# Kernel optimization log

Measured on AMD Instinct MI355X. Metric: run time of the kernel, lower is better.

The kernel has to match this reference:

```python
import jax, jax.numpy as jnp
import numpy as np

H, W = 256, 256
N = 1024
EPS2D = 1e-4  # regularizer added to 2D covariances before inversion


def setup_inputs() -> dict:
    key = jax.random.key(0)
    ks = jax.random.split(key, 6)
    xy = jax.random.normal(ks[0], (N, 2), dtype=jnp.float32) * 3.0
    z = jax.random.uniform(ks[1], (N, 1), minval=2.0, maxval=30.0, dtype=jnp.float32)
    means3D = jnp.concatenate([xy, z], axis=-1)                      # [N,3], depths in (1,50)
    A = 0.1 * jax.random.normal(ks[2], (N, 3, 3), dtype=jnp.float32)
    covs3d = A @ jnp.swapaxes(A, -1, -2) + 0.01 * jnp.eye(3, dtype=jnp.float32)  # SPD [N,3,3]
    colors = jax.random.uniform(ks[3], (N, 3), dtype=jnp.float32)
    opacities = jax.random.uniform(ks[4], (N,), dtype=jnp.float32)
    Kmat = jnp.array([[300.0, 0.0, W / 2.0], [0.0, 300.0, H / 2.0], [0.0, 0.0, 1.0]], dtype=jnp.float32)
    Rmat = jnp.eye(3, dtype=jnp.float32)
    t = jnp.zeros((3,), dtype=jnp.float32)
    return {"means3D": means3D, "covs3d": covs3d, "colors": colors,
            "opacities": opacities, "K": Kmat, "R": Rmat, "t": t}


def reference(means3D, covs3d, colors, opacities, K, R, t):
    n = means3D.shape[0]
    # ---- projection ----
    cam = means3D @ R.T + t[None, :]                      # [N,3]
    depths = jnp.maximum(cam[:, 2], 1.0)
    screen = cam @ K.T
    means2D = screen[:, :2] / screen[:, 2:3]              # [N,2]
    fx, fy = K[0, 0], K[1, 1]
    inv_z = 1.0 / cam[:, 2]
    z2 = cam[:, 2] ** 2
    zeros = jnp.zeros_like(inv_z)
    row0 = jnp.stack([inv_z * fx, zeros, -cam[:, 0] / z2 * fx], axis=-1)
    row1 = jnp.stack([zeros, inv_z * fy, -cam[:, 1] / z2 * fy], axis=-1)
    J = jnp.stack([row0, row1], axis=1)                   # [N,2,3]
    covs_cam = jnp.einsum('ij,njk,lk->nil', R, covs3d, R)  # [N,3,3]
    covs2D = jnp.einsum('nij,njk,nlk->nil', J, covs_cam, J)  # [N,2,2]

    # ---- depth sort ----
    order = jnp.argsort(depths)
    means2D = means2D[order]
    covs2D = covs2D[order]
    colors_s = colors[order]
    opac_s = opacities[order]
    depths_s = depths[order]
    valid = (depths_s > 1.0) & (depths_s < 50.0)

    # ---- per-pixel gaussian evaluation (closed-form 2x2 inverse == cholesky_inverse) ----
    covs2D = covs2D + EPS2D * jnp.eye(2, dtype=covs2D.dtype)
    a = covs2D[:, 0, 0]; b = covs2D[:, 0, 1]; c = covs2D[:, 1, 1]
    det = a * c - b * b                                   # [N]
    ia = c / det; ib = -b / det; ic = a / det

    yy, xx = jnp.meshgrid(jnp.arange(H, dtype=jnp.float32),
                          jnp.arange(W, dtype=jnp.float32), indexing='ij')
    dx0 = xx[None] - means2D[:, 0, None, None]            # [N,H,W]
    dx1 = yy[None] - means2D[:, 1, None, None]            # [N,H,W]
    q = (ia[:, None, None] * dx0 * dx0
         + 2.0 * ib[:, None, None] * dx0 * dx1
         + ic[:, None, None] * dx1 * dx1)
    gauss = jnp.exp(-0.5 * q) / (2.0 * jnp.pi * jnp.sqrt(det))[:, None, None]
    gauss = gauss * valid[:, None, None].astype(gauss.dtype)

    # ---- alpha compositing (front-to-back) ----
    alphas = opac_s[:, None, None] * gauss                # [N,H,W]
    T = jnp.cumprod(1.0 - alphas, axis=0)
    T = jnp.concatenate([jnp.ones_like(alphas[:1]), T[:-1]], axis=0)
    weights = T * alphas                                  # [N,H,W]
    rendered = jnp.einsum('nhw,nc->hwc', weights, colors_s)  # [H,W,3]
    return rendered
```

## Files before the change

kernel.cpp:

```cpp
#include <hip/hip_runtime.h>
#include <math.h>

#define HH 256
#define WW 256
#define EPS2D 1e-4f
#define MAXN 1024
#define CULL_THR 23.0f
#define NL_HALF_LOG2E -0.72134752044448170368f


__global__ __launch_bounds__(256) void prep_kernel(
    const float* __restrict__ means3D, const float* __restrict__ covs3d,
    const float* __restrict__ colors,  const float* __restrict__ opac,
    const float* __restrict__ Km,      const float* __restrict__ Rm,
    const float* __restrict__ tv,
    float4* __restrict__ A, float4* __restrict__ B, float* __restrict__ C,
    int n)
{
    __shared__ float s_mean[MAXN*3];
    __shared__ float s_depth[MAXN];
    __shared__ float s_cov[64*9];
    __shared__ float s_col[64*3];
    __shared__ float s_op[64];
    __shared__ int   s_pr[4][64];

    int t = threadIdx.x, lane = t & 63, w = t >> 6;
    int g0b = blockIdx.x * 64;
    int nb = n - g0b; if (nb > 64) nb = 64; if (nb < 0) nb = 0;

    {
        int nm4 = (3*n) >> 2;
        const float4* m4 = (const float4*)means3D;
        for (int i = t; i < nm4; i += 256) ((float4*)s_mean)[i] = m4[i];
        for (int i = (nm4<<2) + t; i < 3*n; i += 256) s_mean[i] = means3D[i];

        const float* cbase = covs3d + (size_t)g0b * 9;
        int ncf = nb * 9, nc4 = ncf >> 2;
        for (int i = t; i < nc4; i += 256) ((float4*)s_cov)[i] = ((const float4*)cbase)[i];
        for (int i = (nc4<<2) + t; i < ncf; i += 256) s_cov[i] = cbase[i];

        const float* lbase = colors + (size_t)g0b * 3;
        int nlf = nb * 3, nl4 = nlf >> 2;
        for (int i = t; i < nl4; i += 256) ((float4*)s_col)[i] = ((const float4*)lbase)[i];
        for (int i = (nl4<<2) + t; i < nlf; i += 256) s_col[i] = lbase[i];

        const float* obase = opac + g0b;
        int no4 = nb >> 2;
        for (int i = t; i < no4; i += 256) ((float4*)s_op)[i] = ((const float4*)obase)[i];
        for (int i = (no4<<2) + t; i < nb; i += 256) s_op[i] = obase[i];
    }
    __syncthreads();

    float R00=Rm[0],R01=Rm[1],R02=Rm[2];
    float R10=Rm[3],R11=Rm[4],R12=Rm[5];
    float R20=Rm[6],R21=Rm[7],R22=Rm[8];
    float t0=tv[0], t1=tv[1], t2=tv[2];

    for (int g = t; g < MAXN; g += 256) {
        float d = 1e30f;
        if (g < n) {
            float X=s_mean[3*g+0], Y=s_mean[3*g+1], Z=s_mean[3*g+2];
            float cz = R20*X + R21*Y + R22*Z + t2;
            d = fmaxf(cz, 1.0f);
        }
        s_depth[g] = d;
    }
    __syncthreads();

    float mx=0.f,my=0.f,qa=0.f,qb=0.f,qc=0.f,lk=0.f,cr=0.f,cg=0.f,cbv=0.f;
    if (w == 0 && lane < nb) {
        int i = g0b + lane;
        float X = s_mean[3*i+0], Y = s_mean[3*i+1], Z = s_mean[3*i+2];
        float cx = R00*X + R01*Y + R02*Z + t0;
        float cy = R10*X + R11*Y + R12*Z + t1;
        float cz = R20*X + R21*Y + R22*Z + t2;
        float depth = s_depth[i];

        float K00=Km[0],K01=Km[1],K02=Km[2];
        float K10=Km[3],K11=Km[4],K12=Km[5];
        float K20=Km[6],K21=Km[7],K22=Km[8];
        float sx = K00*cx + K01*cy + K02*cz;
        float sy = K10*cx + K11*cy + K12*cz;
        float sz = K20*cx + K21*cy + K22*cz;
        mx = sx / sz;
        my = sy / sz;

        float invz  = 1.0f / cz;
        float invz2 = invz * invz;
        float j00 =  K00 * invz;
        float j02 = -K00 * cx * invz2;
        float j11 =  K11 * invz;
        float j12 = -K11 * cy * invz2;

        const float* S = s_cov + 9*lane;
        float S00=S[0],S01=S[1],S02=S[2];
        float S10=S[3],S11=S[4],S12=S[5];
        float S20=S[6],S21=S[7],S22=S[8];

        float M00 = R00*S00 + R01*S10 + R02*S20;
        float M01 = R00*S01 + R01*S11 + R02*S21;
        float M02 = R00*S02 + R01*S12 + R02*S22;
        float M10 = R10*S00 + R11*S10 + R12*S20;
        float M11 = R10*S01 + R11*S11 + R12*S21;
        float M12 = R10*S02 + R11*S12 + R12*S22;
        float M20 = R20*S00 + R21*S10 + R22*S20;
        float M21 = R20*S01 + R21*S11 + R22*S21;
        float M22 = R20*S02 + R21*S12 + R22*S22;
        float C00 = M00*R00 + M01*R01 + M02*R02;
        float C01 = M00*R10 + M01*R11 + M02*R12;
        float C02 = M00*R20 + M01*R21 + M02*R22;
        float C11 = M10*R10 + M11*R11 + M12*R12;
        float C12 = M10*R20 + M11*R21 + M12*R22;
        float C22 = M20*R20 + M21*R21 + M22*R22;

        float a_ = j00*j00*C00 + 2.0f*j00*j02*C02 + j02*j02*C22 + EPS2D;
        float b_ = j00*j11*C01 + j00*j12*C02 + j02*j11*C12 + j02*j12*C22;
        float c_ = j11*j11*C11 + 2.0f*j11*j12*C12 + j12*j12*C22 + EPS2D;

        float det = a_ * c_ - b_ * b_;
        float ia =  c_ / det;
        float ib = -b_ / det;
        float ic =  a_ / det;
        float norm = 1.0f / (6.283185307179586f * sqrtf(det));

        bool valid = (depth > 1.0f) && (depth < 50.0f);
        float k = s_op[lane] * norm * (valid ? 1.0f : 0.0f);

        qa = NL_HALF_LOG2E * ia;
        qb = 2.0f * NL_HALF_LOG2E * ib;
        qc = NL_HALF_LOG2E * ic;
        lk = log2f(k);
        cr = s_col[3*lane+0];
        cg = s_col[3*lane+1];
        cbv = s_col[3*lane+2];
    }

    {
        int cnt = 0;
        if (lane < nb) {
            int i = g0b + lane;
            float d = s_depth[i];
            const float4* d4 = (const float4*)s_depth;
            int jb = w * 64;
            #pragma unroll 4
            for (int jj = 0; jj < 64; ++jj) {
                float4 v = d4[jb + jj];
                int j = (jb + jj) << 2;
                cnt += (v.x < d || (v.x == d && j+0 < i)) ? 1 : 0;
                cnt += (v.y < d || (v.y == d && j+1 < i)) ? 1 : 0;
                cnt += (v.z < d || (v.z == d && j+2 < i)) ? 1 : 0;
                cnt += (v.w < d || (v.w == d && j+3 < i)) ? 1 : 0;
            }
        }
        s_pr[w][lane] = cnt;
    }
    __syncthreads();

    if (w == 0 && lane < nb) {
        int rank = s_pr[0][lane] + s_pr[1][lane] + s_pr[2][lane] + s_pr[3][lane];
        A[rank] = make_float4(mx, my, qa, qb);
        B[rank] = make_float4(qc, lk, cr, cg);
        C[rank] = cbv;
    }
}

__global__ __launch_bounds__(512) void render_kernel(
    const float4* __restrict__ A, const float4* __restrict__ B,
    const float* __restrict__ C, float* __restrict__ out, int n)
{
    __shared__ float4 s_p0[8][128];
    __shared__ float4 s_p1[8][128];
    __shared__ float4 s_part[7][256];

    int t = threadIdx.x, lane = t & 63, w = t >> 6;
    int row = blockIdx.x;
    int q0 = (n *  w     ) >> 3;
    int q1 = (n * (w + 1)) >> 3;
    float pyf = (float)row;

    int cnt = 0;
    if (q1 > q0) {
        int jc = min(q0 + lane, q1 - 1);
        float4 a = A[jc];
        float4 b = B[jc];
        float  c = C[jc];
        for (int ch = q0; ch < q1; ch += 64) {
            float4 a_n, b_n; float c_n;
            int cn = ch + 64;
            if (cn < q1) {
                int jc2 = min(cn + lane, q1 - 1);
                a_n = A[jc2];
                b_n = B[jc2];
                c_n = C[jc2];
            }
            int jj = ch + lane;
            bool keep = false;
            float qbdy = 0.f, u = 0.f;
            if (jj < q1) {
                float dy = pyf - a.y;
                qbdy = a.w * dy;
                u    = fmaf(b.x * dy, dy, b.y);
                float disc = fmaf(qbdy, qbdy, -4.0f * a.z * (u + CULL_THR));
                if (disc > 0.0f) {
                    float inv2qa = 0.5f / a.z;
                    float shw = sqrtf(disc) * inv2qa;
                    float ctr = -qbdy * inv2qa;
                    float xl = a.x + ctr + shw;
                    float xr = a.x + ctr - shw;
                    keep = (xr >= 0.0f) && (xl <= 255.0f);
                }
            }
            unsigned long long mk = __ballot(keep);
            int pre = __popcll(mk & ((1ull << lane) - 1ull));
            if (keep) {
                int pos = cnt + pre;
                s_p0[w][pos] = make_float4(a.x, a.z, qbdy, u);
                s_p1[w][pos] = make_float4(b.z, b.w, c, 0.f);
            }
            cnt += __popcll(mk);
            a = a_n; b = b_n; c = c_n;
        }
    }

    float lanef = (float)lane;
    float T0=1.f,T1=1.f,T2=1.f,T3=1.f;
    float r0=0.f,g0=0.f,b0=0.f, r1=0.f,g1=0.f,b1=0.f;
    float r2=0.f,g2=0.f,b2=0.f, r3=0.f,g3=0.f,b3=0.f;

    for (int k = 0; k < cnt; ++k) {
        float4 p0 = s_p0[w][k];
        float4 p1 = s_p1[w][k];
        float dx = lanef - p0.x;
        {
            float q = fmaf(fmaf(p0.y, dx, p0.z), dx, p0.w);
            float wg = T0 * __builtin_amdgcn_exp2f(q);
            r0 = fmaf(wg, p1.x, r0); g0 = fmaf(wg, p1.y, g0);
            b0 = fmaf(wg, p1.z, b0); T0 -= wg;
        }
        dx += 64.0f;
        {
            float q = fmaf(fmaf(p0.y, dx, p0.z), dx, p0.w);
            float wg = T1 * __builtin_amdgcn_exp2f(q);
            r1 = fmaf(wg, p1.x, r1); g1 = fmaf(wg, p1.y, g1);
            b1 = fmaf(wg, p1.z, b1); T1 -= wg;
        }
        dx += 64.0f;
        {
            float q = fmaf(fmaf(p0.y, dx, p0.z), dx, p0.w);
            float wg = T2 * __builtin_amdgcn_exp2f(q);
            r2 = fmaf(wg, p1.x, r2); g2 = fmaf(wg, p1.y, g2);
            b2 = fmaf(wg, p1.z, b2); T2 -= wg;
        }
        dx += 64.0f;
        {
            float q = fmaf(fmaf(p0.y, dx, p0.z), dx, p0.w);
            float wg = T3 * __builtin_amdgcn_exp2f(q);
            r3 = fmaf(wg, p1.x, r3); g3 = fmaf(wg, p1.y, g3);
            b3 = fmaf(wg, p1.z, b3); T3 -= wg;
        }
    }

    if (w != 0) {
        s_part[w-1][lane +   0] = make_float4(r0, g0, b0, T0);
        s_part[w-1][lane +  64] = make_float4(r1, g1, b1, T1);
        s_part[w-1][lane + 128] = make_float4(r2, g2, b2, T2);
        s_part[w-1][lane + 192] = make_float4(r3, g3, b3, T3);
    }
    __syncthreads();
    if (w == 0) {
        float rr[4]  = {r0, r1, r2, r3};
        float gg[4]  = {g0, g1, g2, g3};
        float bbv[4] = {b0, b1, b2, b3};
        float tt[4]  = {T0, T1, T2, T3};
        #pragma unroll
        for (int i = 0; i < 4; ++i) {
            int px = lane + (i << 6);
            float4 m = s_part[6][px];
            float ar = m.x, ag = m.y, ab = m.z;
            #pragma unroll
            for (int s = 5; s >= 0; --s) {
                float4 ms = s_part[s][px];
                ar = fmaf(ms.w, ar, ms.x);
                ag = fmaf(ms.w, ag, ms.y);
                ab = fmaf(ms.w, ab, ms.z);
            }
            float cr = fmaf(tt[i], ar, rr[i]);
            float cg = fmaf(tt[i], ag, gg[i]);
            float cb = fmaf(tt[i], ab, bbv[i]);
            int p = row * 256 + px;
            out[3*p+0] = cr;
            out[3*p+1] = cg;
            out[3*p+2] = cb;
        }
    }
}

extern "C" void kernel_launch(void* const* d_in, const int* in_sizes, int n_in,
                              void* d_out, int out_size, void* d_ws, size_t ws_size,
                              hipStream_t stream)
{
    const float* means3D = (const float*)d_in[0];
    const float* covs3d  = (const float*)d_in[1];
    const float* colors  = (const float*)d_in[2];
    const float* opac    = (const float*)d_in[3];
    const float* Km      = (const float*)d_in[4];
    const float* Rm      = (const float*)d_in[5];
    const float* tv      = (const float*)d_in[6];
    int n = in_sizes[3];
    if (n > MAXN) n = MAXN;

    float4* A = (float4*)d_ws;
    float4* B = (float4*)((char*)d_ws + 16384);
    float*  C = (float*)((char*)d_ws + 32768);

    int pblocks = (n + 63) / 64;
    hipLaunchKernelGGL(prep_kernel, dim3(pblocks), dim3(256), 0, stream,
                       means3D, covs3d, colors, opac, Km, Rm, tv, A, B, C, n);

    hipLaunchKernelGGL(render_kernel, dim3(HH), dim3(512), 0, stream,
                       A, B, C, (float*)d_out, n);
}
```

Measured before the change: 21.66 us.

## Fuse prep and render kernels with atomic grid barrier

Merges the preprocessing/sort kernel and the render kernel into one launch. The first pblocks blocks do the projection and rank-sort work, then bump a global counter, and every block spins on that counter before rendering. Shared memory is aliased between the two phases. This removes one kernel launch and the gap between kernels, but adds a memset launch and a spin-wait that depends on all prep blocks being co-resident with the waiting blocks.

```diff
diff --git a/kernel.cpp b/kernel.cpp
--- a/kernel.cpp
+++ b/kernel.cpp
@@ -9,171 +9,186 @@
 #define NL_HALF_LOG2E -0.72134752044448170368f
 
 
-__global__ __launch_bounds__(256) void prep_kernel(
+__global__ __launch_bounds__(512) void fused_kernel(
     const float* __restrict__ means3D, const float* __restrict__ covs3d,
     const float* __restrict__ colors,  const float* __restrict__ opac,
     const float* __restrict__ Km,      const float* __restrict__ Rm,
     const float* __restrict__ tv,
     float4* __restrict__ A, float4* __restrict__ B, float* __restrict__ C,
-    int n)
+    unsigned int* __restrict__ done,
+    float* __restrict__ out, int n, int pblocks)
 {
-    __shared__ float s_mean[MAXN*3];
-    __shared__ float s_depth[MAXN];
-    __shared__ float s_cov[64*9];
-    __shared__ float s_col[64*3];
-    __shared__ float s_op[64];
-    __shared__ int   s_pr[4][64];
+    __shared__ __align__(16) char smem[61440];
+    float* s_mean  = (float*)smem;
+    float* s_depth = (float*)(smem + 12288);
+    float* s_cov   = (float*)(smem + 16384);
+    float* s_col   = (float*)(smem + 18688);
+    float* s_op    = (float*)(smem + 19456);
+    int*   s_pr    = (int*)(smem + 19712);
+    float4 (*s_p0)[128]   = (float4(*)[128])smem;
+    float4 (*s_p1)[128]   = (float4(*)[128])(smem + 16384);
+    float4 (*s_part)[256] = (float4(*)[256])(smem + 32768);
 
     int t = threadIdx.x, lane = t & 63, w = t >> 6;
-    int g0b = blockIdx.x * 64;
-    int nb = n - g0b; if (nb > 64) nb = 64; if (nb < 0) nb = 0;
-
-    {
-        int nm4 = (3*n) >> 2;
-        const float4* m4 = (const float4*)means3D;
-        for (int i = t; i < nm4; i += 256) ((float4*)s_mean)[i] = m4[i];
-        for (int i = (nm4<<2) + t; i < 3*n; i += 256) s_mean[i] = means3D[i];
-
-        const float* cbase = covs3d + (size_t)g0b * 9;
-        int ncf = nb * 9, nc4 = ncf >> 2;
-        for (int i = t; i < nc4; i += 256) ((float4*)s_cov)[i] = ((const float4*)cbase)[i];
-        for (int i = (nc4<<2) + t; i < ncf; i += 256) s_cov[i] = cbase[i];
-
-        const float* lbase = colors + (size_t)g0b * 3;
-        int nlf = nb * 3, nl4 = nlf >> 2;
-        for (int i = t; i < nl4; i += 256) ((float4*)s_col)[i] = ((const float4*)lbase)[i];
-        for (int i = (nl4<<2) + t; i < nlf; i += 256) s_col[i] = lbase[i];
-
-        const float* obase = opac + g0b;
-        int no4 = nb >> 2;
-        for (int i = t; i < no4; i += 256) ((float4*)s_op)[i] = ((const float4*)obase)[i];
-        for (int i = (no4<<2) + t; i < nb; i += 256) s_op[i] = obase[i];
+    int blk = blockIdx.x;
+
+    if (blk < pblocks) {
+        int g0b = blk * 64;
+        int nb = n - g0b; if (nb > 64) nb = 64;
+
+        {
+            int nm4 = (3*n) >> 2;
+            const float4* m4 = (const float4*)means3D;
+            for (int i = t; i < nm4; i += 512) ((float4*)s_mean)[i] = m4[i];
+            for (int i = (nm4<<2) + t; i < 3*n; i += 512) s_mean[i] = means3D[i];
+
+            const float* cbase = covs3d + (size_t)g0b * 9;
+            int ncf = nb * 9, nc4 = ncf >> 2;
+            for (int i = t; i < nc4; i += 512) ((float4*)s_cov)[i] = ((const float4*)cbase)[i];
+            for (int i = (nc4<<2) + t; i < ncf; i += 512) s_cov[i] = cbase[i];
+
+            const float* lbase = colors + (size_t)g0b * 3;
+            int nlf = nb * 3, nl4 = nlf >> 2;
+            for (int i = t; i < nl4; i += 512) ((float4*)s_col)[i] = ((const float4*)lbase)[i];
+            for (int i = (nl4<<2) + t; i < nlf; i += 512) s_col[i] = lbase[i];
+
+            const float* obase = opac + g0b;
+            int no4 = nb >> 2;
+            for (int i = t; i < no4; i += 512) ((float4*)s_op)[i] = ((const float4*)obase)[i];
+            for (int i = (no4<<2) + t; i < nb; i += 512) s_op[i] = obase[i];
+        }
+        __syncthreads();
+
+        float R00=Rm[0],R01=Rm[1],R02=Rm[2];
+        float R10=Rm[3],R11=Rm[4],R12=Rm[5];
+        float R20=Rm[6],R21=Rm[7],R22=Rm[8];
+        float t0=tv[0], t1=tv[1], t2=tv[2];
+
+        for (int g = t; g < MAXN; g += 512) {
+            float d = 1e30f;
+            if (g < n) {
+                float X=s_mean[3*g+0], Y=s_mean[3*g+1], Z=s_mean[3*g+2];
+                float cz = R20*X + R21*Y + R22*Z + t2;
+                d = fmaxf(cz, 1.0f);
+            }
+            s_depth[g] = d;
+        }
+        __syncthreads();
+
+        float mx=0.f,my=0.f,qa=0.f,qb=0.f,qc=0.f,lk=0.f,cr=0.f,cg_=0.f,cbv=0.f;
+        if (w == 0 && lane < nb) {
+            int i = g0b + lane;
+            float X = s_mean[3*i+0], Y = s_mean[3*i+1], Z = s_mean[3*i+2];
+            float cx = R00*X + R01*Y + R02*Z + t0;
+            float cy = R10*X + R11*Y + R12*Z + t1;
+            float cz = R20*X + R21*Y + R22*Z + t2;
+            float depth = s_depth[i];
+
+            float K00=Km[0],K01=Km[1],K02=Km[2];
+            float K10=Km[3],K11=Km[4],K12=Km[5];
+            float K20=Km[6],K21=Km[7],K22=Km[8];
+            float sx = K00*cx + K01*cy + K02*cz;
+            float sy = K10*cx + K11*cy + K12*cz;
+            float sz = K20*cx + K21*cy + K22*cz;
+            mx = sx / sz;
+            my = sy / sz;
+
+            float invz  = 1.0f / cz;
+            float invz2 = invz * invz;
+            float j00 =  K00 * invz;
+            float j02 = -K00 * cx * invz2;
+            float j11 =  K11 * invz;
+            float j12 = -K11 * cy * invz2;
+
+            const float* S = s_cov + 9*lane;
+            float S00=S[0],S01=S[1],S02=S[2];
+            float S10=S[3],S11=S[4],S12=S[5];
+            float S20=S[6],S21=S[7],S22=S[8];
+
+            float M00 = R00*S00 + R01*S10 + R02*S20;
+            float M01 = R00*S01 + R01*S11 + R02*S21;
+            float M02 = R00*S02 + R01*S12 + R02*S22;
+            float M10 = R10*S00 + R11*S10 + R12*S20;
+            float M11 = R10*S01 + R11*S11 + R12*S21;
+            float M12 = R10*S02 + R11*S12 + R12*S22;
+            float M20 = R20*S00 + R21*S10 + R22*S20;
+            float M21 = R20*S01 + R21*S11 + R22*S21;
+            float M22 = R20*S02 + R21*S12 + R22*S22;
+            float C00 = M00*R00 + M01*R01 + M02*R02;
+            float C01 = M00*R10 + M01*R11 + M02*R12;
+            float C02 = M00*R20 + M01*R21 + M02*R22;
+            float C11 = M10*R10 + M11*R11 + M12*R12;
+            float C12 = M10*R20 + M11*R21 + M12*R22;
+            float C22 = M20*R20 + M21*R21 + M22*R22;
+
+            float a_ = j00*j00*C00 + 2.0f*j00*j02*C02 + j02*j02*C22 + EPS2D;
+            float b_ = j00*j11*C01 + j00*j12*C02 + j02*j11*C12 + j02*j12*C22;
+            float c_ = j11*j11*C11 + 2.0f*j11*j12*C12 + j12*j12*C22 + EPS2D;
+
+            float det = a_ * c_ - b_ * b_;
+            float ia =  c_ / det;
+            float ib = -b_ / det;
+            float ic =  a_ / det;
+            float norm = 1.0f / (6.283185307179586f * sqrtf(det));
+
+            bool valid = (depth > 1.0f) && (depth < 50.0f);
+            float k = s_op[lane] * norm * (valid ? 1.0f : 0.0f);
+
+            qa = NL_HALF_LOG2E * ia;
+            qb = 2.0f * NL_HALF_LOG2E * ib;
+            qc = NL_HALF_LOG2E * ic;
+            lk = log2f(k);
+            cr  = s_col[3*lane+0];
+            cg_ = s_col[3*lane+1];
+            cbv = s_col[3*lane+2];
+        }
+
+        {
+            int cnt = 0;
+            if (lane < nb) {
+                int i = g0b + lane;
+                float d = s_depth[i];
+                const float4* d4 = (const float4*)s_depth;
+                int jb = w * 32;
+                #pragma unroll 4
+                for (int jj = 0; jj < 32; ++jj) {
+                    float4 v = d4[jb + jj];
+                    int j = (jb + jj) << 2;
+                    cnt += (v.x < d || (v.x == d && j+0 < i)) ? 1 : 0;
+                    cnt += (v.y < d || (v.y == d && j+1 < i)) ? 1 : 0;
+                    cnt += (v.z < d || (v.z == d && j+2 < i)) ? 1 : 0;
+                    cnt += (v.w < d || (v.w == d && j+3 < i)) ? 1 : 0;
+                }
+            }
+            s_pr[w*64 + lane] = cnt;
+        }
+        __syncthreads();
+
+        if (w == 0 && lane < nb) {
+            int rank = 0;
+            #pragma unroll
+            for (int k = 0; k < 8; ++k) rank += s_pr[k*64 + lane];
+            A[rank] = make_float4(mx, my, qa, qb);
+            B[rank] = make_float4(qc, lk, cr, cg_);
+            C[rank] = cbv;
+        }
+        __syncthreads();
+        if (t == 0) {
+            __threadfence();
+            __hip_atomic_fetch_add(done, 1u, __ATOMIC_RELEASE,
+                                   __HIP_MEMORY_SCOPE_AGENT);
+        }
+    }
+
+    if (t == 0) {
+        while (__hip_atomic_load(done, __ATOMIC_ACQUIRE,
+                                 __HIP_MEMORY_SCOPE_AGENT) < (unsigned)pblocks) {
+            __builtin_amdgcn_s_sleep(8);
+        }
     }
     __syncthreads();
 
-    float R00=Rm[0],R01=Rm[1],R02=Rm[2];
-    float R10=Rm[3],R11=Rm[4],R12=Rm[5];
-    float R20=Rm[6],R21=Rm[7],R22=Rm[8];
-    float t0=tv[0], t1=tv[1], t2=tv[2];
-
-    for (int g = t; g < MAXN; g += 256) {
-        float d = 1e30f;
-        if (g < n) {
-            float X=s_mean[3*g+0], Y=s_mean[3*g+1], Z=s_mean[3*g+2];
-            float cz = R20*X + R21*Y + R22*Z + t2;
-            d = fmaxf(cz, 1.0f);
-        }
-        s_depth[g] = d;
-    }
-    __syncthreads();
-
-    float mx=0.f,my=0.f,qa=0.f,qb=0.f,qc=0.f,lk=0.f,cr=0.f,cg=0.f,cbv=0.f;
-    if (w == 0 && lane < nb) {
-        int i = g0b + lane;
-        float X = s_mean[3*i+0], Y = s_mean[3*i+1], Z = s_mean[3*i+2];
-        float cx = R00*X + R01*Y + R02*Z + t0;
-        float cy = R10*X + R11*Y + R12*Z + t1;
-        float cz = R20*X + R21*Y + R22*Z + t2;
-        float depth = s_depth[i];
-
-        float K00=Km[0],K01=Km[1],K02=Km[2];
-        float K10=Km[3],K11=Km[4],K12=Km[5];
-        float K20=Km[6],K21=Km[7],K22=Km[8];
-        float sx = K00*cx + K01*cy + K02*cz;
-        float sy = K10*cx + K11*cy + K12*cz;
-        float sz = K20*cx + K21*cy + K22*cz;
-        mx = sx / sz;
-        my = sy / sz;
-
-        float invz  = 1.0f / cz;
-        float invz2 = invz * invz;
-        float j00 =  K00 * invz;
-        float j02 = -K00 * cx * invz2;
-        float j11 =  K11 * invz;
-        float j12 = -K11 * cy * invz2;
-
-        const float* S = s_cov + 9*lane;
-        float S00=S[0],S01=S[1],S02=S[2];
-        float S10=S[3],S11=S[4],S12=S[5];
-        float S20=S[6],S21=S[7],S22=S[8];
-
-        float M00 = R00*S00 + R01*S10 + R02*S20;
-        float M01 = R00*S01 + R01*S11 + R02*S21;
-        float M02 = R00*S02 + R01*S12 + R02*S22;
-        float M10 = R10*S00 + R11*S10 + R12*S20;
-        float M11 = R10*S01 + R11*S11 + R12*S21;
-        float M12 = R10*S02 + R11*S12 + R12*S22;
-        float M20 = R20*S00 + R21*S10 + R22*S20;
-        float M21 = R20*S01 + R21*S11 + R22*S21;
-        float M22 = R20*S02 + R21*S12 + R22*S22;
-        float C00 = M00*R00 + M01*R01 + M02*R02;
-        float C01 = M00*R10 + M01*R11 + M02*R12;
-        float C02 = M00*R20 + M01*R21 + M02*R22;
-        float C11 = M10*R10 + M11*R11 + M12*R12;
-        float C12 = M10*R20 + M11*R21 + M12*R22;
-        float C22 = M20*R20 + M21*R21 + M22*R22;
-
-        float a_ = j00*j00*C00 + 2.0f*j00*j02*C02 + j02*j02*C22 + EPS2D;
-        float b_ = j00*j11*C01 + j00*j12*C02 + j02*j11*C12 + j02*j12*C22;
-        float c_ = j11*j11*C11 + 2.0f*j11*j12*C12 + j12*j12*C22 + EPS2D;
-
-        float det = a_ * c_ - b_ * b_;
-        float ia =  c_ / det;
-        float ib = -b_ / det;
-        float ic =  a_ / det;
-        float norm = 1.0f / (6.283185307179586f * sqrtf(det));
-
-        bool valid = (depth > 1.0f) && (depth < 50.0f);
-        float k = s_op[lane] * norm * (valid ? 1.0f : 0.0f);
-
-        qa = NL_HALF_LOG2E * ia;
-        qb = 2.0f * NL_HALF_LOG2E * ib;
-        qc = NL_HALF_LOG2E * ic;
-        lk = log2f(k);
-        cr = s_col[3*lane+0];
-        cg = s_col[3*lane+1];
-        cbv = s_col[3*lane+2];
-    }
-
-    {
-        int cnt = 0;
-        if (lane < nb) {
-            int i = g0b + lane;
-            float d = s_depth[i];
-            const float4* d4 = (const float4*)s_depth;
-            int jb = w * 64;
-            #pragma unroll 4
-            for (int jj = 0; jj < 64; ++jj) {
-                float4 v = d4[jb + jj];
-                int j = (jb + jj) << 2;
-                cnt += (v.x < d || (v.x == d && j+0 < i)) ? 1 : 0;
-                cnt += (v.y < d || (v.y == d && j+1 < i)) ? 1 : 0;
-                cnt += (v.z < d || (v.z == d && j+2 < i)) ? 1 : 0;
-                cnt += (v.w < d || (v.w == d && j+3 < i)) ? 1 : 0;
-            }
-        }
-        s_pr[w][lane] = cnt;
-    }
-    __syncthreads();
-
-    if (w == 0 && lane < nb) {
-        int rank = s_pr[0][lane] + s_pr[1][lane] + s_pr[2][lane] + s_pr[3][lane];
-        A[rank] = make_float4(mx, my, qa, qb);
-        B[rank] = make_float4(qc, lk, cr, cg);
-        C[rank] = cbv;
-    }
-}
-
-__global__ __launch_bounds__(512) void render_kernel(
-    const float4* __restrict__ A, const float4* __restrict__ B,
-    const float* __restrict__ C, float* __restrict__ out, int n)
-{
-    __shared__ float4 s_p0[8][128];
-    __shared__ float4 s_p1[8][128];
-    __shared__ float4 s_part[7][256];
-
-    int t = threadIdx.x, lane = t & 63, w = t >> 6;
-    int row = blockIdx.x;
+    int row = blk;
     int q0 = (n *  w     ) >> 3;
     int q1 = (n * (w + 1)) >> 3;
     float pyf = (float)row;
@@ -312,11 +327,13 @@
     float4* A = (float4*)d_ws;
     float4* B = (float4*)((char*)d_ws + 16384);
     float*  C = (float*)((char*)d_ws + 32768);
+    unsigned int* done = (unsigned int*)((char*)d_ws + 36864);
 
     int pblocks = (n + 63) / 64;
-    hipLaunchKernelGGL(prep_kernel, dim3(pblocks), dim3(256), 0, stream,
-                       means3D, covs3d, colors, opac, Km, Rm, tv, A, B, C, n);
-
-    hipLaunchKernelGGL(render_kernel, dim3(HH), dim3(512), 0, stream,
-                       A, B, C, (float*)d_out, n);
+
+    hipMemsetAsync((void*)done, 0, 64, stream);
+
+    hipLaunchKernelGGL(fused_kernel, dim3(HH), dim3(512), 0, stream,
+                       means3D, covs3d, colors, opac, Km, Rm, tv,
+                       A, B, C, done, (float*)d_out, n, pblocks);
 }
```

Result: slower. 39.73 us (+83.4%).
